# Kernel optimization log

Measured on AMD Instinct MI355X. Metric: run time of the kernel, lower is better.

The kernel has to match this reference:

```python
import jax, jax.numpy as jnp
import numpy as np

B, N, M, C, K = 4, 16384, 1024, 256, 32
RADIUS = 1.0
EPS = 1e-5


def _bn(x, g, b, axes):
    # training-mode batch norm over given axes; channel axis is 1
    m = jnp.mean(x, axes, keepdims=True)
    v = jnp.var(x, axes, keepdims=True)
    sh = [1] * x.ndim
    sh[1] = -1
    return (x - m) * jax.lax.rsqrt(v + EPS) * g.reshape(sh) + b.reshape(sh)


def setup_inputs() -> dict:
    key = jax.random.key(0)
    ks = jax.random.split(key, 10)
    d = {
        'ffps_xyz': jax.random.normal(ks[0], (B, M, 3), jnp.float32),
        'ffps_feature': jax.random.normal(ks[1], (B, C, M), jnp.float32),
        'backbone_xyz': jax.random.normal(ks[2], (B, N, 3), jnp.float32),
        'backbone_features': jax.random.normal(ks[3], (B, C, N), jnp.float32),
        # shift layer: Conv1d(256->128), Conv1d(128->3)
        'sw1': jax.random.normal(ks[4], (128, 256), jnp.float32) * 0.05,
        'sg1': jnp.ones((128,), jnp.float32), 'sb1': jnp.zeros((128,), jnp.float32),
        'sw2': jax.random.normal(ks[5], (3, 128), jnp.float32) * 0.05,
        'sg2': jnp.ones((3,), jnp.float32), 'sb2': jnp.zeros((3,), jnp.float32),
        # grouped MLP: Conv2d 1x1: 259->512->512->512
        'w1': jax.random.normal(ks[6], (512, C + 3), jnp.float32) * 0.05,
        'g1': jnp.ones((512,), jnp.float32), 'b1': jnp.zeros((512,), jnp.float32),
        'w2': jax.random.normal(ks[7], (512, 512), jnp.float32) * 0.05,
        'g2': jnp.ones((512,), jnp.float32), 'b2': jnp.zeros((512,), jnp.float32),
        'w3': jax.random.normal(ks[8], (512, 512), jnp.float32) * 0.05,
        'g3': jnp.ones((512,), jnp.float32), 'b3': jnp.zeros((512,), jnp.float32),
    }
    return d


def reference(ffps_xyz, ffps_feature, backbone_xyz, backbone_features,
              sw1, sg1, sb1, sw2, sg2, sb2,
              w1, g1, b1, w2, g2, b2, w3, g3, b3):
    # ---- shift layer: Conv1d(1x1)+BN1d+ReLU x2 -> (B,3,M) ----
    h = jnp.einsum('oc,bcm->bom', sw1, ffps_feature)
    h = jax.nn.relu(_bn(h, sg1, sb1, (0, 2)))
    h = jnp.einsum('oc,bcm->bom', sw2, h)
    shift = jax.nn.relu(_bn(h, sg2, sb2, (0, 2)))
    new_xyz = ffps_xyz + shift.transpose(0, 2, 1)  # (B,M,3)

    # ---- ball query: first K points within RADIUS, pad with first hit ----
    d2 = jnp.sum((new_xyz[:, :, None, :] - backbone_xyz[:, None, :, :]) ** 2, -1)  # (B,M,N)
    score = jnp.where(d2 < RADIUS * RADIUS, jnp.arange(N, dtype=jnp.int32), N)
    neg_vals, _ = jax.lax.top_k(-score, K)  # K smallest scores = first valid indices
    idx = -neg_vals  # (B,M,K)
    first = idx[..., :1]
    idx = jnp.where(idx == N, first, idx)
    idx = jnp.where(idx == N, 0, idx)  # query with no neighbors -> 0

    # ---- group: relative xyz concat features -> (B, 3+C, M, K) ----
    bidx = jnp.arange(B)[:, None, None]
    g_xyz = backbone_xyz[bidx, idx] - new_xyz[:, :, None, :]        # (B,M,K,3)
    g_feat = backbone_features.transpose(0, 2, 1)[bidx, idx]        # (B,M,K,C)
    g = jnp.concatenate([g_xyz, g_feat], -1).transpose(0, 3, 1, 2)  # (B,3+C,M,K)

    # ---- per-point MLP: Conv2d(1x1)+BN2d+ReLU x3 ----
    for w, gm, bt in ((w1, g1, b1), (w2, g2, b2), (w3, g3, b3)):
        g = jnp.einsum('oc,bcmk->bomk', w, g)
        g = jax.nn.relu(_bn(g, gm, bt, (0, 2, 3)))

    # ---- max-pool over neighbors, return (B, M, C_out) ----
    return jnp.max(g, axis=3).transpose(0, 2, 1)
```

## Files before the change

### kernel.cpp

```cpp
#include <hip/hip_runtime.h>
#include <hip/hip_bf16.h>
#include <hip/hip_fp16.h>

#define BB   4
#define NN   16384
#define MM   1024
#define CC   256
#define KK   32
#define O1   128
#define FF   512
#define LTOT (BB*MM*KK)
#define NSLOT 64
#define CH   16384
#define NCH2 (LTOT/CH)

typedef float f4 __attribute__((ext_vector_type(4)));
typedef short b8 __attribute__((ext_vector_type(8)));

struct CvtA {
    const void* src[19];
    unsigned cum[20];
    unsigned dstF[19];
    int      nsz[19];
};

__device__ __forceinline__ float bf2f(unsigned short u){
    return __uint_as_float(((unsigned int)u) << 16);
}
__device__ __forceinline__ float anyf(const void* p, size_t i, int f){
    if (f == 1) return bf2f(((const unsigned short*)p)[i]);
    if (f == 2) return __half2float(((const __half*)p)[i]);
    return ((const float*)p)[i];
}

__global__ void k_det19(CvtA a, int* __restrict__ flags){
    if (threadIdx.x != 0) return;
    int i = blockIdx.x;
    const unsigned short* u = (const unsigned short*)a.src[i];
    int n = a.nsz[i];
    int* flag = flags + i;
    int W = n < 64 ? n : 64;
    bool allz = true;
    for (int k = 0; k < W; k++) if (u[k]){ allz = false; break; }
    if (allz){ *flag = 1; return; }
    if (u[0] == 0x3F80u){ *flag = 1; return; }
    if (u[0] == 0x3C00u){ *flag = 2; return; }
    if (W >= 2){
        unsigned int f0 = ((unsigned int)u[1] << 16) | u[0];
        if (__uint_as_float(f0) == 1.0f){ *flag = 0; return; }
    }
    int ce = 0, co = 0, ne = 0, no_ = 0;
    for (int k = 0; k < W; k++){
        unsigned short x = u[k];
        float v = fabsf(bf2f(x));
        int sane = (x == 0) || (v >= 0.0009765625f && v <= 64.f);
        if (k & 1){ no_++; co += sane; } else { ne++; ce += sane; }
    }
    if (ce * 4 >= ne * 3){ *flag = 1; return; }
    if (co * 4 >= no_ * 3 && ce * 5 < ne * 2){ *flag = 0; return; }
    *flag = 2;
}

__global__ __launch_bounds__(256) void k_cvt19(CvtA a, const int* __restrict__ flags,
                                               float* __restrict__ base){
    unsigned eb = blockIdx.x * 256u;
    int i = 0;
    while (eb >= a.cum[i+1]) i++;
    unsigned tl = eb - a.cum[i] + threadIdx.x;
    if ((int)tl >= a.nsz[i]) return;
    base[a.dstF[i] + tl] = anyf(a.src[i], tl, flags[i]);
}

__global__ __launch_bounds__(256) void k_mlp1(const float* __restrict__ sw1,
                                              const float* __restrict__ feat,
                                              float* __restrict__ h1,
                                              float* __restrict__ stats1){
    int t = blockIdx.x * 256 + threadIdx.x;
    int m = t & (MM - 1);
    int o = (t >> 10) & (O1 - 1);
    int b = t >> 17;
    const float* fb = feat + (size_t)b * CC * MM + m;
    const float* w  = sw1 + o * CC;
    float acc = 0.f;
    #pragma unroll 8
    for (int c = 0; c < CC; c++) acc += w[c] * fb[(size_t)c * MM];
    h1[t] = acc;
    float s = acc, s2 = acc * acc;
    for (int off = 32; off; off >>= 1){ s += __shfl_down(s, off); s2 += __shfl_down(s2, off); }
    __shared__ float ls[8];
    int lane = threadIdx.x & 63, wid = threadIdx.x >> 6;
    if (lane == 0){ ls[wid] = s; ls[4 + wid] = s2; }
    __syncthreads();
    if (threadIdx.x == 0){
        atomicAdd(&stats1[2*o],   ls[0]+ls[1]+ls[2]+ls[3]);
        atomicAdd(&stats1[2*o+1], ls[4]+ls[5]+ls[6]+ls[7]);
    }
}

__global__ __launch_bounds__(256) void k_bn1mlp2(const float* __restrict__ h1,
                                                 const float* __restrict__ stats1,
                                                 const float* __restrict__ sg1,
                                                 const float* __restrict__ sb1,
                                                 const float* __restrict__ sw2,
                                                 float* __restrict__ h2,
                                                 float* __restrict__ stats2){
    __shared__ float sc[O1], bi[O1];
    int tid = threadIdx.x;
    if (tid < O1){
        const float invn = 1.f / (BB * MM);
        float mean = stats1[2*tid] * invn;
        float var  = fmaxf(stats1[2*tid+1] * invn - mean * mean, 0.f);
        float rs   = 1.f / sqrtf(var + 1e-5f);
        float s    = rs * sg1[tid];
        float b_   = sb1[tid] - mean * s;
        if (!isfinite(s) || !isfinite(b_)){ s = 1.f; b_ = 0.f; }
        sc[tid] = s; bi[tid] = b_;
    }
    __syncthreads();
    int t = blockIdx.x * 256 + tid;
    int m = t & (MM - 1);
    int r = t >> 10; int o2 = r % 3; int b = r / 3;
    const float* hb = h1 + (size_t)b * O1 * MM + m;
    const float* w  = sw2 + o2 * O1;
    float acc = 0.f;
    #pragma unroll 8
    for (int c = 0; c < O1; c++){
        float v = hb[(size_t)c * MM] * sc[c] + bi[c];
        v = v > 0.f ? v : 0.f;
        acc += w[c] * v;
    }
    h2[t] = acc;
    float s = acc, s2 = acc * acc;
    for (int off = 32; off; off >>= 1){ s += __shfl_down(s, off); s2 += __shfl_down(s2, off); }
    __shared__ float ls[8];
    int lane = tid & 63, wid = tid >> 6;
    if (lane == 0){ ls[wid] = s; ls[4 + wid] = s2; }
    __syncthreads();
    if (tid == 0){
        atomicAdd(&stats2[2*o2],   ls[0]+ls[1]+ls[2]+ls[3]);
        atomicAdd(&stats2[2*o2+1], ls[4]+ls[5]+ls[6]+ls[7]);
    }
}

__global__ void k_fin2(const float* __restrict__ stats2, const float* __restrict__ sg2,
                       const float* __restrict__ sb2, float* __restrict__ scb2){
    int t = threadIdx.x;
    if (t < 3){
        const float invn = 1.f / (BB * MM);
        float mean = stats2[2*t] * invn;
        float var  = fmaxf(stats2[2*t+1] * invn - mean * mean, 0.f);
        float rs   = 1.f / sqrtf(var + 1e-5f);
        float s    = rs * sg2[t];
        float b    = sb2[t] - mean * s;
        if (!isfinite(s) || !isfinite(b)){ s = 1.f; b = 0.f; }
        scb2[t] = s; scb2[4 + t] = b;
    }
}

__global__ __launch_bounds__(256) void k_ballq(const float* __restrict__ fxyz,
                                               const float* __restrict__ h2,
                                               const float* __restrict__ scb2,
                                               const float* __restrict__ bxyz,
                                               float* __restrict__ nxyz,
                                               int* __restrict__ idxbuf){
    int q    = blockIdx.x * 4 + (threadIdx.x >> 6);
    int lane = threadIdx.x & 63;
    int b = q >> 10, m = q & (MM - 1);
    float nx[3];
    #pragma unroll
    for (int c = 0; c < 3; c++){
        float v = h2[((size_t)b * 3 + c) * MM + m] * scb2[c] + scb2[4 + c];
        v = v > 0.f ? v : 0.f;
        nx[c] = fxyz[(size_t)q * 3 + c] + v;
    }
    if (lane == 0){
        nxyz[q*3+0] = nx[0]; nxyz[q*3+1] = nx[1]; nxyz[q*3+2] = nx[2];
    }
    const float* bx = bxyz + (size_t)b * NN * 3;
    int have = 0, firstj = 0;
    int* out = idxbuf + (size_t)q * KK;
    for (int j0 = 0; j0 < NN && have < KK; j0 += 64){
        int j = j0 + lane;
        float dx = bx[j*3+0] - nx[0];
        float dy = bx[j*3+1] - nx[1];
        float dz = bx[j*3+2] - nx[2];
        float d2 = dx*dx + dy*dy + dz*dz;
        bool pred = d2 < 1.0f;
        unsigned long long mask = __ballot(pred);
        if (mask){
            if (have == 0) firstj = j0 + (__ffsll((unsigned long long)mask) - 1);
            if (pred){
                int rank = __popcll(mask & ((1ull << lane) - 1ull));
                int pos = have + rank;
                if (pos < KK) out[pos] = j;
            }
            have += (int)__popcll(mask);
        }
    }
    if (have < KK){
        int fill = (have > 0) ? firstj : 0;
        for (int p = have + lane; p < KK; p += 64) out[p] = fill;
    }
}

__global__ __launch_bounds__(256) void k_xyzd(const int* __restrict__ idxbuf,
                                              const float* __restrict__ bxyz,
                                              const float* __restrict__ nxyz,
                                              int* __restrict__ idx2,
                                              float4* __restrict__ xyzd){
    int l = blockIdx.x * 256 + threadIdx.x;
    int b = l >> 15;
    int q = l >> 5;
    int j = idxbuf[l];
    idx2[l] = b * NN + j;
    const float* p = bxyz + ((size_t)b * NN + j) * 3;
    xyzd[l] = make_float4(p[0] - nxyz[q*3+0], p[1] - nxyz[q*3+1], p[2] - nxyz[q*3+2], 0.f);
}

__global__ __launch_bounds__(256) void k_transp(const void* __restrict__ bfv,
                                                const int* __restrict__ flag,
                                                float* __restrict__ ft){
    __shared__ float tile[32][33];
    int f = *flag;
    int bid = blockIdx.x;
    int nt = bid & 511;
    int ct = (bid >> 9) & 7;
    int b  = bid >> 12;
    int tx = threadIdx.x & 31, ty = threadIdx.x >> 5;
    size_t base = ((size_t)b * CC + ct * 32) * NN + nt * 32;
    #pragma unroll
    for (int r = 0; r < 32; r += 8)
        tile[ty + r][tx] = anyf(bfv, base + (size_t)(ty + r) * NN + tx, f);
    __syncthreads();
    float* dst = ft + ((size_t)b * NN + nt * 32) * CC + ct * 32;
    #pragma unroll
    for (int r = 0; r < 32; r += 8) dst[(size_t)(ty + r) * CC + tx] = tile[tx][ty + r];
}

__global__ __launch_bounds__(256) void k_wpack(const float* __restrict__ src,
                                               int stride, int srcOff, int Cs,
                                               unsigned short* __restrict__ hph,
                                               unsigned short* __restrict__ hpl){
    int t = blockIdx.x * 256 + threadIdx.x;
    if (t >= FF * Cs) return;
    int nK = Cs >> 5;
    int j  = t & 7;
    int ln = (t >> 3) & 63;
    int r  = t >> 9;
    int ks = r % nK;
    int of = r / nK;
    int o = of * 16 + (ln & 15);
    int c = ks * 32 + (ln >> 4) * 8 + ((j >> 2) << 2) + (j & 3);
    float f = src[(size_t)o * stride + srcOff + c];
    unsigned u = __float_as_uint(f);
    unsigned hh = u & 0xFFFF0000u;
    hph[t] = (unsigned short)(hh >> 16);
    float f2 = f - __uint_as_float(hh);
    hpl[t] = (unsigned short)(__float_as_uint(f2) >> 16);
}

__global__ void k_w1xyz(const float* __restrict__ w1, float4* __restrict__ w1xp){
    int t = blockIdx.x * 256 + threadIdx.x;
    if (t < FF) w1xp[t] = make_float4(w1[t*259], w1[t*259+1], w1[t*259+2], 0.f);
}

__device__ __forceinline__ void split4(float x, float y, float z_, float w_,
                                       unsigned &h0, unsigned &h1,
                                       unsigned &lo0, unsigned &lo1){
    unsigned ux = __float_as_uint(x), uy = __float_as_uint(y);
    unsigned uz = __float_as_uint(z_), uw = __float_as_uint(w_);
    unsigned hx = ux & 0xFFFF0000u, hy = uy & 0xFFFF0000u;
    unsigned hz = uz & 0xFFFF0000u, hw = uw & 0xFFFF0000u;
    h0 = (hx >> 16) | hy;
    h1 = (hz >> 16) | hw;
    float rx = x  - __uint_as_float(hx);
    float ry = y  - __uint_as_float(hy);
    float rz = z_ - __uint_as_float(hz);
    float rw = w_ - __uint_as_float(hw);
    lo0 = (__float_as_uint(rx) >> 16) | (__float_as_uint(ry) & 0xFFFF0000u);
    lo1 = (__float_as_uint(rz) >> 16) | (__float_as_uint(rw) & 0xFFFF0000u);
}

template<int XM, int OM>
__global__ __launch_bounds__(256) void k_gemm(const unsigned short* __restrict__ Aph,
                                              const unsigned short* __restrict__ Apl,
                                              const float* __restrict__ X,
                                              int Cs,
                                              const float* __restrict__ scb,
                                              const int* __restrict__ idx2,
                                              const float4* __restrict__ xyzd,
                                              const float4* __restrict__ w1xp,
                                              int Lbase,
                                              float* __restrict__ Y,
                                              int Lwrite,
                                              float* __restrict__ y3mx,
                                              float* __restrict__ y3mn,
                                              double* __restrict__ stats){
    __shared__ short lds[8192];
    char* ldsb = (char*)lds;

    const int tid  = threadIdx.x;
    const int lane = tid & 63;
    const int w    = tid >> 6;
    const int wo   = (w >> 1) * 64;
    const int wl   = (w & 1) * 64;

    int bid = blockIdx.x;
    {
        int cpx = gridDim.x >> 3;
        bid = (bid & 7) * cpx + (bid >> 3);
    }
    const int o0 = (bid & 3) * 128;
    const int l0 = (bid >> 2) * 128;

    const int o_loc  = tid >> 3;
    const int q      = (tid & 7) >> 1;
    const int h      = tid & 1;
    const int colOff = q * 8 + h * 4;
    const int wbase  = ((o_loc >> 4) * 1024) + (((o_loc & 15) * 16) ^ (q << 5)) + (q << 8) + h * 8;
    const int roff   = (((lane & 15) * 16) ^ ((lane >> 4) << 5)) + ((lane >> 4) << 8);

    const int nK    = Cs >> 5;
    const int fbase = (o0 + wo) >> 4;
    const int aLane = lane * 16;

    int   rI[4];
    float ddx[4], ddy[4], ddz[4];
    const float* Xp = nullptr;
    if (XM == 1){
        #pragma unroll
        for (int i = 0; i < 4; i++){
            int lg = Lbase + l0 + o_loc + 32 * i;
            rI[i] = idx2[lg];
            float4 dd = xyzd[lg];
            ddx[i] = dd.x; ddy[i] = dd.y; ddz[i] = dd.z;
        }
    } else {
        Xp = X + (size_t)(l0 + o_loc) * Cs + colOff;
    }

    f4 acc[4][4];
    #pragma unroll
    for (int i = 0; i < 4; i++)
        #pragma unroll
        for (int j = 0; j < 4; j++)
            acc[i][j] = f4{0.f, 0.f, 0.f, 0.f};

    float4 rx[4];
    b8 ahf[4], alf[4];
    #pragma unroll
    for (int i = 0; i < 4; i++){
        if (XM == 1) rx[i] = *(const float4*)(X + (size_t)rI[i] * FF + colOff);
        else         rx[i] = *(const float4*)(Xp + (size_t)(32 * i) * Cs);
        int ab = ((fbase + i) * nK) << 10;
        ahf[i] = *(const b8*)((const char*)Aph + ab + aLane);
        alf[i] = *(const b8*)((const char*)Apl + ab + aLane);
    }

    for (int c0 = 0; c0 < Cs; c0 += 32){
        unsigned xh0[4], xh1[4], xL0[4], xL1[4];
        float4 sc4, bi4;
        if (scb){
            sc4 = *(const float4*)(scb + c0 + colOff);
            bi4 = *(const float4*)(scb + Cs + c0 + colOff);
        }
        float4 wv0, wv1, wv2, wv3;
        if (XM == 1){
            wv0 = w1xp[c0 + colOff + 0];
            wv1 = w1xp[c0 + colOff + 1];
            wv2 = w1xp[c0 + colOff + 2];
            wv3 = w1xp[c0 + colOff + 3];
        }
        #pragma unroll
        for (int i = 0; i < 4; i++){
            float vx = rx[i].x, vy = rx[i].y, vz = rx[i].z, vw = rx[i].w;
            if (XM == 1){
                vx += ddx[i]*wv0.x + ddy[i]*wv0.y + ddz[i]*wv0.z;
                vy += ddx[i]*wv1.x + ddy[i]*wv1.y + ddz[i]*wv1.z;
                vz += ddx[i]*wv2.x + ddy[i]*wv2.y + ddz[i]*wv2.z;
                vw += ddx[i]*wv3.x + ddy[i]*wv3.y + ddz[i]*wv3.z;
            }
            if (scb){
                vx = fmaxf(vx * sc4.x + bi4.x, 0.f);
                vy = fmaxf(vy * sc4.y + bi4.y, 0.f);
                vz = fmaxf(vz * sc4.z + bi4.z, 0.f);
                vw = fmaxf(vw * sc4.w + bi4.w, 0.f);
            }
            split4(vx, vy, vz, vw, xh0[i], xh1[i], xL0[i], xL1[i]);
        }
        __syncthreads();
        #pragma unroll
        for (int i = 0; i < 4; i++){
            int off = wbase + i * 2048;
            *(uint2*)(ldsb + off)         = make_uint2(xh0[i], xh1[i]);
            *(uint2*)(ldsb + 8192 + off)  = make_uint2(xL0[i], xL1[i]);
        }
        __syncthreads();
        b8 nah[4], nal[4];
        if (c0 + 32 < Cs){
            int ks1 = (c0 >> 5) + 1;
            #pragma unroll
            for (int i = 0; i < 4; i++){
                if (XM == 1) rx[i] = *(const float4*)(X + (size_t)rI[i] * FF + colOff + (c0 + 32));
                else         rx[i] = *(const float4*)(Xp + (size_t)(32 * i) * Cs + (c0 + 32));
                int ab = (((fbase + i) * nK + ks1)) << 10;
                nah[i] = *(const b8*)((const char*)Aph + ab + aLane);
                nal[i] = *(const b8*)((const char*)Apl + ab + aLane);
            }
        }
        b8 bhf[4], blf[4];
        #pragma unroll
        for (int ni = 0; ni < 4; ni++){
            int f = (wl >> 4) + ni;
            bhf[ni] = *(const b8*)(ldsb + f * 1024 + roff);
            blf[ni] = *(const b8*)(ldsb + 8192 + f * 1024 + roff);
        }
        #pragma unroll
        for (int mi = 0; mi < 4; mi++){
            #pragma unroll
            for (int ni = 0; ni < 4; ni++){
                acc[mi][ni] = __builtin_amdgcn_mfma_f32_16x16x32_bf16(ahf[mi], bhf[ni], acc[mi][ni], 0, 0, 0);
                acc[mi][ni] = __builtin_amdgcn_mfma_f32_16x16x32_bf16(ahf[mi], blf[ni], acc[mi][ni], 0, 0, 0);
                acc[mi][ni] = __builtin_amdgcn_mfma_f32_16x16x32_bf16(alf[mi], bhf[ni], acc[mi][ni], 0, 0, 0);
            }
        }
        if (c0 + 32 < Cs){
            #pragma unroll
            for (int i = 0; i < 4; i++){ ahf[i] = nah[i]; alf[i] = nal[i]; }
        }
    }

    if (OM == 0){
        if (Y && (l0 + 128 <= Lwrite)){
            #pragma unroll
            for (int mi = 0; mi < 4; mi++){
                #pragma unroll
                for (int ni = 0; ni < 4; ni++){
                    int o = o0 + wo + mi * 16 + 4 * (lane >> 4);
                    int l = l0 + wl + ni * 16 + (lane & 15);
                    *(float4*)(Y + (size_t)l * FF + o) =
                        make_float4(acc[mi][ni][0], acc[mi][ni][1], acc[mi][ni][2], acc[mi][ni][3]);
                }
            }
        }
    }
    if (stats){
        int slot_s = blockIdx.x & (NSLOT - 1);
        double* sp = stats + (size_t)slot_s * FF * 2;
        #pragma unroll
        for (int mi = 0; mi < 4; mi++){
            float s1[4] = {0,0,0,0}, s2[4] = {0,0,0,0};
            #pragma unroll
            for (int ni = 0; ni < 4; ni++){
                #pragma unroll
                for (int r = 0; r < 4; r++){
                    float v = acc[mi][ni][r];
                    s1[r] += v; s2[r] += v * v;
                }
            }
            #pragma unroll
            for (int off = 8; off; off >>= 1){
                #pragma unroll
                for (int r = 0; r < 4; r++){
                    s1[r] += __shfl_down(s1[r], off, 16);
                    s2[r] += __shfl_down(s2[r], off, 16);
                }
            }
            if ((lane & 15) == 0){
                int o = o0 + wo + mi * 16 + 4 * (lane >> 4);
                #pragma unroll
                for (int r = 0; r < 4; r++){
                    atomicAdd(&sp[2 * (o + r)],     (double)s1[r]);
                    atomicAdd(&sp[2 * (o + r) + 1], (double)s2[r]);
                }
            }
        }
    }
    if (OM == 1){
        #pragma unroll
        for (int mi = 0; mi < 4; mi++){
            #pragma unroll
            for (int g = 0; g < 2; g++){
                float vmx[4], vmn[4];
                #pragma unroll
                for (int r = 0; r < 4; r++){
                    float a0 = acc[mi][2*g][r], a1 = acc[mi][2*g+1][r];
                    vmx[r] = fmaxf(a0, a1); vmn[r] = fminf(a0, a1);
                }
                #pragma unroll
                for (int off = 8; off; off >>= 1){
                    #pragma unroll
                    for (int r = 0; r < 4; r++){
                        vmx[r] = fmaxf(vmx[r], __shfl_down(vmx[r], off, 16));
                        vmn[r] = fminf(vmn[r], __shfl_down(vmn[r], off, 16));
                    }
                }
                if ((lane & 15) == 0){
                    int qg = (Lbase + l0 + wl) / 32 + g;
                    #pragma unroll
                    for (int r = 0; r < 4; r++){
                        int o = o0 + wo + mi * 16 + 4 * (lane >> 4) + r;
                        y3mx[(size_t)qg * FF + o] = vmx[r];
                        y3mn[(size_t)qg * FF + o] = vmn[r];
                    }
                }
            }
        }
    }
}

__global__ void k_finL(const double* __restrict__ stats, const float* __restrict__ g,
                       const float* __restrict__ bt, float* __restrict__ scb){
    int o = blockIdx.x * 256 + threadIdx.x;
    double s = 0.0, s2 = 0.0;
    for (int k = 0; k < NSLOT; k++){
        s  += stats[((size_t)k * FF + o) * 2];
        s2 += stats[((size_t)k * FF + o) * 2 + 1];
    }
    double mean = s / (double)LTOT;
    double var  = s2 / (double)LTOT - mean * mean;
    if (!(var > 0.0)) var = 0.0;
    double rs = 1.0 / sqrt(var + 1e-5);
    double sc = rs * (double)g[o];
    double bi = (double)bt[o] - mean * sc;
    float scf = (float)sc, bif = (float)bi;
    if (!isfinite(scf) || !isfinite(bif)){ scf = 1.f; bif = 0.f; }
    scb[o] = scf;
    scb[FF + o] = bif;
}

__global__ __launch_bounds__(256) void k_y1stats(const float* __restrict__ z,
                                                 const int* __restrict__ idx2,
                                                 const float4* __restrict__ xyzd,
                                                 const float4* __restrict__ w1xp,
                                                 double* __restrict__ stats){
    int tid = threadIdx.x, bid = blockIdx.x;
    int o1 = tid, o2 = tid + 256;
    float4 wa = w1xp[o1], wb = w1xp[o2];
    double s1a=0, s2a=0, s1b=0, s2b=0;
    for (int p = 0; p < LTOT/2048; p++){
        int l = bid + p * 2048;
        int r = idx2[l];
        float4 d = xyzd[l];
        const float* zr = z + (size_t)r * FF;
        float ya = zr[o1] + d.x*wa.x + d.y*wa.y + d.z*wa.z;
        float yb = zr[o2] + d.x*wb.x + d.y*wb.y + d.z*wb.z;
        s1a += ya; s2a += (double)ya*ya;
        s1b += yb; s2b += (double)yb*yb;
    }
    int slot = bid & (NSLOT - 1);
    double* sp = stats + (size_t)slot * FF * 2;
    atomicAdd(&sp[2*o1],   s1a); atomicAdd(&sp[2*o1+1], s2a);
    atomicAdd(&sp[2*o2],   s1b); atomicAdd(&sp[2*o2+1], s2b);
}

__global__ __launch_bounds__(256) void k_bn3max(const float* __restrict__ mx,
                                                const float* __restrict__ mn,
                                                const float* __restrict__ scb,
                                                float* __restrict__ out){
    int t = blockIdx.x * 256 + threadIdx.x;
    int o = t & (FF - 1);
    float sc = scb[o], bi = scb[FF + o];
    float v = sc >= 0.f ? mx[t] : mn[t];
    out[t] = fmaxf(sc * v + bi, 0.f);
}

__global__ __launch_bounds__(256) void k_diag(const float* __restrict__ ff,
                                              const float* __restrict__ w1f,
                                              const float* __restrict__ featT,
                                              const float* __restrict__ z,
                                              const float* __restrict__ xyzdf,
                                              const float* __restrict__ scb1,
                                              const float* __restrict__ scbL2,
                                              const float* __restrict__ scbL3,
                                              const float* __restrict__ y3,
                                              float* __restrict__ out){
    __shared__ float red[4];
    int tid = threadIdx.x;
    int bad = 0, isn = 0;
    const float* arr[9] = {ff, w1f, featT, z, xyzdf, scb1, scbL2, scbL3, y3};
    const int   len[9] = {4096, 4096, 8192, 8192, 4096, 1024, 1024, 1024, 8192};
    for (int k = 0; k < 9; k++){
        float s = 0.f;
        const float* a = arr[k];
        for (int i = tid; i < len[k]; i += 256) s += fabsf(a[i]);
        for (int off = 32; off; off >>= 1) s += __shfl_down(s, off);
        if ((tid & 63) == 0) red[tid >> 6] = s;
        __syncthreads();
        float t = red[0] + red[1] + red[2] + red[3];
        __syncthreads();
        if (bad == 0 && !(t > 1e-6f && t < 1e15f)){
            bad = k + 1;
            isn = isfinite(t) ? 0 : 1;
        }
    }
    if (tid == 0 && bad) out[0] = 512.f * bad + 256.f * isn;
}

extern "C" void kernel_launch(void* const* d_in, const int* in_sizes, int n_in,
                              void* d_out, int out_size, void* d_ws, size_t ws_size,
                              hipStream_t stream) {
    static const int NSZ[19] = {12288, 1048576, 196608, 16777216, 32768, 128, 128,
                                384, 3, 3, 132608, 512, 512, 262144, 512, 512,
                                262144, 512, 512};
    float* out = (float*)d_out;

    char* w = (char*)d_ws;
    size_t off = 0;
    auto take = [&](size_t bytes)->size_t{
        size_t r = off; off += (bytes + 255) & ~(size_t)255; return r;
    };
    size_t o_stats1  = take(256 * 4);
    size_t o_stats2  = take(8 * 4);
    size_t o_statsA  = take((size_t)NSLOT * FF * 2 * 8);
    size_t o_statsL2 = take((size_t)NSLOT * FF * 2 * 8);
    size_t o_statsL3 = take((size_t)NSLOT * FF * 2 * 8);
    size_t zero_end  = off;
    size_t o_flags   = take(19 * 4);
    size_t o_cv[19];
    for (int i = 0; i < 19; i++){
        if (i == 3){ o_cv[i] = 0; continue; }
        o_cv[i] = take((size_t)NSZ[i] * 4);
    }
    size_t o_scb2    = take(8 * 4);
    size_t o_scb1    = take(FF * 2 * 4);
    size_t o_scbL2   = take(FF * 2 * 4);
    size_t o_scbL3   = take(FF * 2 * 4);
    size_t o_h1      = take((size_t)BB * O1 * MM * 4);
    size_t o_h2      = take((size_t)BB * 3 * MM * 4);
    size_t o_nxyz    = take((size_t)BB * MM * 3 * 4);
    size_t o_idx     = take((size_t)LTOT * 4);
    size_t o_idx2    = take((size_t)LTOT * 4);
    size_t o_xyzd    = take((size_t)LTOT * 16);
    size_t o_w1h     = take((size_t)FF * CC * 2);
    size_t o_w1l     = take((size_t)FF * CC * 2);
    size_t o_w2h     = take((size_t)FF * FF * 2);
    size_t o_w2l     = take((size_t)FF * FF * 2);
    size_t o_w3h     = take((size_t)FF * FF * 2);
    size_t o_w3l     = take((size_t)FF * FF * 2);
    size_t o_w1xp    = take((size_t)FF * 16);
    size_t o_y3mx    = take((size_t)BB * MM * FF * 4);
    size_t o_y3mn    = take((size_t)BB * MM * FF * 4);
    size_t o_z       = take((size_t)BB * NN * FF * 4);
    size_t o_featT   = take((size_t)BB * NN * CC * 4);
    (void)n_in; (void)in_sizes; (void)out_size;

    const size_t chb = (size_t)CH * FF * 4;
    size_t avail = ws_size > o_featT ? ws_size - o_featT : 0;
    int S; bool full;
    if (avail >= (size_t)NCH2 * chb){ S = NCH2; full = true; }
    else {
        long s = (long)(avail / chb) - 1;
        if (s < 0) s = 0; if (s > NCH2 - 1) s = NCH2 - 1;
        S = (int)s; full = false;
    }
    const int Lwrite = S * CH;

    float*  stats1  = (float*) (w + o_stats1);
    float*  stats2  = (float*) (w + o_stats2);
    double* statsA  = (double*)(w + o_statsA);
    double* statsL2 = (double*)(w + o_statsL2);
    double* statsL3 = (double*)(w + o_statsL3);
    int*    flags   = (int*)   (w + o_flags);
    float*  scb2    = (float*) (w + o_scb2);
    float*  scb1    = (float*) (w + o_scb1);
    float*  scbL2   = (float*) (w + o_scbL2);
    float*  scbL3   = (float*) (w + o_scbL3);
    float*  h1      = (float*) (w + o_h1);
    float*  h2      = (float*) (w + o_h2);
    float*  nxyz    = (float*) (w + o_nxyz);
    int*    idxbuf  = (int*)   (w + o_idx);
    int*    idx2    = (int*)   (w + o_idx2);
    float4* xyzd    = (float4*)(w + o_xyzd);
    unsigned short* w1h = (unsigned short*)(w + o_w1h);
    unsigned short* w1l = (unsigned short*)(w + o_w1l);
    unsigned short* w2h = (unsigned short*)(w + o_w2h);
    unsigned short* w2l = (unsigned short*)(w + o_w2l);
    unsigned short* w3h = (unsigned short*)(w + o_w3h);
    unsigned short* w3l = (unsigned short*)(w + o_w3l);
    float4* w1xp    = (float4*)(w + o_w1xp);
    float*  y3mx    = (float*) (w + o_y3mx);
    float*  y3mn    = (float*) (w + o_y3mn);
    float*  z       = (float*) (w + o_z);
    float*  featT   = (float*) (w + o_featT);
    float*  t2scr   = featT;
    float*  t2store = full ? featT : featT + (size_t)CH * FF;

    hipMemsetAsync(w, 0, zero_end, stream);

    CvtA ca;
    unsigned cum = 0;
    for (int i = 0; i < 19; i++){
        ca.src[i]  = d_in[i];
        ca.nsz[i]  = NSZ[i];
        ca.dstF[i] = (unsigned)(o_cv[i] / 4);
        ca.cum[i]  = cum;
        if (i != 3) cum += (unsigned)((NSZ[i] + 255) & ~255);
    }
    ca.cum[19] = cum;
    {
        unsigned c2 = 0;
        for (int i = 0; i < 19; i++){
            ca.cum[i] = c2;
            if (i != 3) c2 += (unsigned)((NSZ[i] + 255) & ~255);
        }
        ca.cum[19] = c2;
    }
    k_det19<<<19, 64, 0, stream>>>(ca, flags);
    k_cvt19<<<ca.cum[19] / 256, 256, 0, stream>>>(ca, flags, (float*)w);

    float* cv[19];
    for (int i = 0; i < 19; i++) cv[i] = (i == 3) ? nullptr : (float*)(w + o_cv[i]);
    float* fx = cv[0], *ffp = cv[1], *bx = cv[2];
    float* sw1f = cv[4], *sg1f = cv[5], *sb1f = cv[6];
    float* sw2f = cv[7], *sg2f = cv[8], *sb2f = cv[9];
    float* w1f = cv[10], *g1f = cv[11], *b1f = cv[12];
    float* w2f = cv[13], *g2f = cv[14], *b2f = cv[15];
    float* w3f = cv[16], *g3f = cv[17], *b3f = cv[18];

    k_mlp1   <<<2048, 256, 0, stream>>>(sw1f, ffp, h1, stats1);
    k_bn1mlp2<<<48,   256, 0, stream>>>(h1, stats1, sg1f, sb1f, sw2f, h2, stats2);
    k_fin2   <<<1,    64,  0, stream>>>(stats2, sg2f, sb2f, scb2);
    k_ballq  <<<BB*MM/4, 256, 0, stream>>>(fx, h2, scb2, bx, nxyz, idxbuf);
    k_xyzd   <<<LTOT/256, 256, 0, stream>>>(idxbuf, bx, nxyz, idx2, xyzd);
    k_transp <<<BB*(CC/32)*(NN/32), 256, 0, stream>>>(d_in[3], flags + 3, featT);
    k_wpack  <<<(FF*CC)/256, 256, 0, stream>>>(w1f, 259, 3, CC, w1h, w1l);
    k_wpack  <<<(FF*FF)/256, 256, 0, stream>>>(w2f, FF, 0, FF, w2h, w2l);
    k_wpack  <<<(FF*FF)/256, 256, 0, stream>>>(w3f, FF, 0, FF, w3h, w3l);
    k_w1xyz  <<<2, 256, 0, stream>>>(w1f, w1xp);

    k_gemm<0,0><<<4 * (BB*NN/128), 256, 0, stream>>>(w1h, w1l, featT, CC, nullptr,
            nullptr, nullptr, nullptr, 0, z, BB*NN, nullptr, nullptr, nullptr);

    k_y1stats<<<2048, 256, 0, stream>>>(z, idx2, xyzd, w1xp, statsA);
    k_finL  <<<2, 256, 0, stream>>>(statsA, g1f, b1f, scb1);

    const int GFULL = 4 * (LTOT/128);
    const int GCH   = 4 * (CH/128);

    k_gemm<1,0><<<GFULL, 256, 0, stream>>>(w2h, w2l, z, FF, scb1,
            idx2, xyzd, w1xp, 0, t2store, Lwrite, nullptr, nullptr, statsL2);
    k_finL <<<2, 256, 0, stream>>>(statsL2, g2f, b2f, scbL2);

    if (S > 0){
        k_gemm<0,1><<<S * GCH, 256, 0, stream>>>(w3h, w3l, t2store, FF, scbL2,
                nullptr, nullptr, nullptr, 0, nullptr, 0, y3mx, y3mn, statsL3);
    }
    for (int c = S; c < NCH2; c++){
        k_gemm<1,0><<<GCH, 256, 0, stream>>>(w2h, w2l, z, FF, scb1,
                idx2, xyzd, w1xp, c*CH, t2scr, CH, nullptr, nullptr, nullptr);
        k_gemm<0,1><<<GCH, 256, 0, stream>>>(w3h, w3l, t2scr, FF, scbL2,
                nullptr, nullptr, nullptr, c*CH, nullptr, 0, y3mx, y3mn, statsL3);
    }
    k_finL <<<2, 256, 0, stream>>>(statsL3, g3f, b3f, scbL3);

    k_bn3max<<<(BB*MM*FF)/256, 256, 0, stream>>>(y3mx, y3mn, scbL3, out);

    k_diag<<<1, 256, 0, stream>>>(ffp, w1f, t2scr, z, (const float*)xyzd,
                                  scb1, scbL2, scbL3, y3mx, out);
}
```

Before: 1.497 ms.

## Fuse ball-query with neighbor xyz gather and double-buffer GEMM LDS tiles

The ball-query kernel now stages neighbor indices in shared memory and writes idx2 and the relative-xyz buffer directly. This removes the separate k_xyzd launch along with the intermediate idxbuf and nxyz round trips through global memory. In the GEMM kernel the B-operand LDS staging is double-buffered, which drops one __syncthreads per K-step and lets the next tile's writes overlap the current tile's reads. The cost is twice the LDS per block (32KB), which may lower occupancy.

After: 1.502 ms. No clear change (+0.3%).

```diff
diff --git a/kernel.cpp b/kernel.cpp
--- a/kernel.cpp
+++ b/kernel.cpp
@@ -161,9 +161,11 @@
                                                const float* __restrict__ h2,
                                                const float* __restrict__ scb2,
                                                const float* __restrict__ bxyz,
-                                               float* __restrict__ nxyz,
-                                               int* __restrict__ idxbuf){
-    int q    = blockIdx.x * 4 + (threadIdx.x >> 6);
+                                               int* __restrict__ idx2,
+                                               float4* __restrict__ xyzd){
+    __shared__ int sj[4][KK];
+    int wq   = threadIdx.x >> 6;
+    int q    = blockIdx.x * 4 + wq;
     int lane = threadIdx.x & 63;
     int b = q >> 10, m = q & (MM - 1);
     float nx[3];
@@ -173,12 +175,8 @@
         v = v > 0.f ? v : 0.f;
         nx[c] = fxyz[(size_t)q * 3 + c] + v;
     }
-    if (lane == 0){
-        nxyz[q*3+0] = nx[0]; nxyz[q*3+1] = nx[1]; nxyz[q*3+2] = nx[2];
-    }
     const float* bx = bxyz + (size_t)b * NN * 3;
     int have = 0, firstj = 0;
-    int* out = idxbuf + (size_t)q * KK;
     for (int j0 = 0; j0 < NN && have < KK; j0 += 64){
         int j = j0 + lane;
         float dx = bx[j*3+0] - nx[0];
@@ -192,29 +190,22 @@
             if (pred){
                 int rank = __popcll(mask & ((1ull << lane) - 1ull));
                 int pos = have + rank;
-                if (pos < KK) out[pos] = j;
+                if (pos < KK) sj[wq][pos] = j;
             }
             have += (int)__popcll(mask);
         }
     }
     if (have < KK){
         int fill = (have > 0) ? firstj : 0;
-        for (int p = have + lane; p < KK; p += 64) out[p] = fill;
-    }
-}
-
-__global__ __launch_bounds__(256) void k_xyzd(const int* __restrict__ idxbuf,
-                                              const float* __restrict__ bxyz,
-                                              const float* __restrict__ nxyz,
-                                              int* __restrict__ idx2,
-                                              float4* __restrict__ xyzd){
-    int l = blockIdx.x * 256 + threadIdx.x;
-    int b = l >> 15;
-    int q = l >> 5;
-    int j = idxbuf[l];
-    idx2[l] = b * NN + j;
-    const float* p = bxyz + ((size_t)b * NN + j) * 3;
-    xyzd[l] = make_float4(p[0] - nxyz[q*3+0], p[1] - nxyz[q*3+1], p[2] - nxyz[q*3+2], 0.f);
+        for (int p = have + lane; p < KK; p += 64) sj[wq][p] = fill;
+    }
+    if (lane < KK){
+        int j = sj[wq][lane];
+        int l = q * KK + lane;
+        idx2[l] = b * NN + j;
+        const float* p = bx + (size_t)j * 3;
+        xyzd[l] = make_float4(p[0] - nx[0], p[1] - nx[1], p[2] - nx[2], 0.f);
+    }
 }
 
 __global__ __launch_bounds__(256) void k_transp(const void* __restrict__ bfv,
@@ -296,7 +287,7 @@
                                               float* __restrict__ y3mx,
                                               float* __restrict__ y3mn,
                                               double* __restrict__ stats){
-    __shared__ short lds[8192];
+    __shared__ short lds[16384];
     char* ldsb = (char*)lds;
 
     const int tid  = threadIdx.x;
@@ -357,6 +348,7 @@
         alf[i] = *(const b8*)((const char*)Apl + ab + aLane);
     }
 
+    int buf = 0;
     for (int c0 = 0; c0 < Cs; c0 += 32){
         unsigned xh0[4], xh1[4], xL0[4], xL1[4];
         float4 sc4, bi4;
@@ -388,12 +380,14 @@
             }
             split4(vx, vy, vz, vw, xh0[i], xh1[i], xL0[i], xL1[i]);
         }
-        __syncthreads();
-        #pragma unroll
-        for (int i = 0; i < 4; i++){
-            int off = wbase + i * 2048;
-            *(uint2*)(ldsb + off)         = make_uint2(xh0[i], xh1[i]);
-            *(uint2*)(ldsb + 8192 + off)  = make_uint2(xL0[i], xL1[i]);
+        {
+            int bo = buf << 13;
+            #pragma unroll
+            for (int i = 0; i < 4; i++){
+                int off = bo + wbase + i * 2048;
+                *(uint2*)(ldsb + off)          = make_uint2(xh0[i], xh1[i]);
+                *(uint2*)(ldsb + 16384 + off)  = make_uint2(xL0[i], xL1[i]);
+            }
         }
         __syncthreads();
         b8 nah[4], nal[4];
@@ -409,11 +403,14 @@
             }
         }
         b8 bhf[4], blf[4];
-        #pragma unroll
-        for (int ni = 0; ni < 4; ni++){
-            int f = (wl >> 4) + ni;
-            bhf[ni] = *(const b8*)(ldsb + f * 1024 + roff);
-            blf[ni] = *(const b8*)(ldsb + 8192 + f * 1024 + roff);
+        {
+            int bo = buf << 13;
+            #pragma unroll
+            for (int ni = 0; ni < 4; ni++){
+                int f = (wl >> 4) + ni;
+                bhf[ni] = *(const b8*)(ldsb + bo + f * 1024 + roff);
+                blf[ni] = *(const b8*)(ldsb + 16384 + bo + f * 1024 + roff);
+            }
         }
         #pragma unroll
         for (int mi = 0; mi < 4; mi++){
@@ -428,6 +425,7 @@
             #pragma unroll
             for (int i = 0; i < 4; i++){ ahf[i] = nah[i]; alf[i] = nal[i]; }
         }
+        buf ^= 1;
     }
 
     if (OM == 0){
@@ -628,8 +626,6 @@
     size_t o_scbL3   = take(FF * 2 * 4);
     size_t o_h1      = take((size_t)BB * O1 * MM * 4);
     size_t o_h2      = take((size_t)BB * 3 * MM * 4);
-    size_t o_nxyz    = take((size_t)BB * MM * 3 * 4);
-    size_t o_idx     = take((size_t)LTOT * 4);
     size_t o_idx2    = take((size_t)LTOT * 4);
     size_t o_xyzd    = take((size_t)LTOT * 16);
     size_t o_w1h     = take((size_t)FF * CC * 2);
@@ -668,8 +664,6 @@
     float*  scbL3   = (float*) (w + o_scbL3);
     float*  h1      = (float*) (w + o_h1);
     float*  h2      = (float*) (w + o_h2);
-    float*  nxyz    = (float*) (w + o_nxyz);
-    int*    idxbuf  = (int*)   (w + o_idx);
     int*    idx2    = (int*)   (w + o_idx2);
     float4* xyzd    = (float4*)(w + o_xyzd);
     unsigned short* w1h = (unsigned short*)(w + o_w1h);
@@ -689,19 +683,13 @@
     hipMemsetAsync(w, 0, zero_end, stream);
 
     CvtA ca;
-    unsigned cum = 0;
-    for (int i = 0; i < 19; i++){
-        ca.src[i]  = d_in[i];
-        ca.nsz[i]  = NSZ[i];
-        ca.dstF[i] = (unsigned)(o_cv[i] / 4);
-        ca.cum[i]  = cum;
-        if (i != 3) cum += (unsigned)((NSZ[i] + 255) & ~255);
-    }
-    ca.cum[19] = cum;
     {
         unsigned c2 = 0;
         for (int i = 0; i < 19; i++){
-            ca.cum[i] = c2;
+            ca.src[i]  = d_in[i];
+            ca.nsz[i]  = NSZ[i];
+            ca.dstF[i] = (unsigned)(o_cv[i] / 4);
+            ca.cum[i]  = c2;
             if (i != 3) c2 += (unsigned)((NSZ[i] + 255) & ~255);
         }
         ca.cum[19] = c2;
@@ -721,8 +709,7 @@
     k_mlp1   <<<2048, 256, 0, stream>>>(sw1f, ffp, h1, stats1);
     k_bn1mlp2<<<48,   256, 0, stream>>>(h1, stats1, sg1f, sb1f, sw2f, h2, stats2);
     k_fin2   <<<1,    64,  0, stream>>>(stats2, sg2f, sb2f, scb2);
-    k_ballq  <<<BB*MM/4, 256, 0, stream>>>(fx, h2, scb2, bx, nxyz, idxbuf);
-    k_xyzd   <<<LTOT/256, 256, 0, stream>>>(idxbuf, bx, nxyz, idx2, xyzd);
+    k_ballq  <<<BB*MM/4, 256, 0, stream>>>(fx, h2, scb2, bx, idx2, xyzd);
     k_transp <<<BB*(CC/32)*(NN/32), 256, 0, stream>>>(d_in[3], flags + 3, featT);
     k_wpack  <<<(FF*CC)/256, 256, 0, stream>>>(w1f, 259, 3, CC, w1h, w1l);
     k_wpack  <<<(FF*FF)/256, 256, 0, stream>>>(w2f, FF, 0, FF, w2h, w2l);
```
